# Kernel tuning notes

Hardware: AMD Instinct MI355X
Metric: run time of the kernel (lower is better)

## Reference

```python
import jax, jax.numpy as jnp
import numpy as np

NUM_NODES = 1_000_000
D_IN = 128
D_OUT = 128
NUM_REL = 16          # relations; +1 for self-connection relation
BATCH = 16384
NUM_SAMPLE = 32


def setup_inputs() -> dict:
    key = jax.random.key(0)
    k1, k2, k3, k4 = jax.random.split(key, 4)
    embed_table = jax.random.normal(k1, (NUM_NODES, D_IN), dtype=jnp.float32)
    # per-relation weight: [R+1, size_out, size_in], xavier-ish scale
    relation_weights = jax.random.normal(k2, (NUM_REL + 1, D_OUT, D_IN), dtype=jnp.float32)
    relation_weights = relation_weights * jnp.sqrt(2.0 / (D_IN + D_OUT))
    sampled_neighbors = jax.random.randint(k3, (BATCH, NUM_SAMPLE), 0, NUM_NODES, dtype=jnp.int64)
    sampled_relations = jax.random.randint(k4, (BATCH, NUM_SAMPLE), 0, NUM_REL + 1, dtype=jnp.int64)
    return {
        "embed_table": embed_table,
        "relation_weights": relation_weights,
        "sampled_neighbors": sampled_neighbors,
        "sampled_relations": sampled_relations,
    }


def reference(embed_table, relation_weights, sampled_neighbors, sampled_relations):
    # Gather sampled neighbor embeddings: [N, S, D]
    emb = embed_table[sampled_neighbors]
    num_sample = emb.shape[1]
    num_rel_p1 = relation_weights.shape[0]
    # One-hot relation mask [N, S, R+1]; aggregated = mean over S of (emb * onehot)
    # Equivalent einsum avoids materializing the [N, S, R+1, D] intermediate.
    onehot = jax.nn.one_hot(sampled_relations, num_rel_p1, dtype=emb.dtype)
    agg = jnp.einsum("nsr,nsd->nrd", onehot, emb) / num_sample  # [N, R+1, D]
    # Per-relation matmul (bmm over R+1) then mean over relations.
    # relation_weights: [R+1, O, I]; agg: [N, R+1, I] -> [N, O]
    out = jnp.einsum("nri,roi->no", agg, relation_weights) / num_rel_p1
    return jax.nn.relu(out * 1000.0)
```

## Files before the change

### kernel.cpp

```cpp
#include <hip/hip_runtime.h>

constexpr int D     = 128;
constexpr int R1    = 17;
constexpr int BATCH = 16384;
constexpr int S     = 32;
constexpr int K     = R1 * D;
constexpr int KB    = K / 8;
constexpr int NPB   = 16;
constexpr int AS    = K + 8;
constexpr int THREADS = 512;

typedef __attribute__((ext_vector_type(8))) short short8;
typedef __attribute__((ext_vector_type(4))) float f32x4;

__device__ __forceinline__ unsigned short f2bf_u(float f) {
    union { float f; unsigned u; } c; c.f = f;
    unsigned u = c.u;
    u += 0x7fffu + ((u >> 16) & 1u);
    return (unsigned short)(u >> 16);
}

__device__ __forceinline__ unsigned pack2bf(float lo, float hi) {
    return (unsigned)f2bf_u(lo) | ((unsigned)f2bf_u(hi) << 16);
}

__global__ void pack_w_kernel(const float* __restrict__ W, short* __restrict__ Bp) {
    int tid = blockIdx.x * 256 + threadIdx.x;
    if (tid >= R1 * D * D) return;
    int og = tid / K;
    int k  = tid - og * K;
    int r = k >> 7, i = k & 127;
    float v = W[((size_t)r * D + og) * D + i];
    int ot = og >> 4, o = og & 15, kb = k >> 3, j = k & 7;
    Bp[(((size_t)ot * KB + kb) * 16 + o) * 8 + j] = (short)f2bf_u(v);
}

#define ACC_SWITCH(r, x)                                              \
    switch (r) {                                                      \
        case 0:  a0.x  += x.x; a0.y  += x.y; break;                   \
        case 1:  a1.x  += x.x; a1.y  += x.y; break;                   \
        case 2:  a2.x  += x.x; a2.y  += x.y; break;                   \
        case 3:  a3.x  += x.x; a3.y  += x.y; break;                   \
        case 4:  a4.x  += x.x; a4.y  += x.y; break;                   \
        case 5:  a5.x  += x.x; a5.y  += x.y; break;                   \
        case 6:  a6.x  += x.x; a6.y  += x.y; break;                   \
        case 7:  a7.x  += x.x; a7.y  += x.y; break;                   \
        case 8:  a8.x  += x.x; a8.y  += x.y; break;                   \
        case 9:  a9.x  += x.x; a9.y  += x.y; break;                   \
        case 10: a10.x += x.x; a10.y += x.y; break;                   \
        case 11: a11.x += x.x; a11.y += x.y; break;                   \
        case 12: a12.x += x.x; a12.y += x.y; break;                   \
        case 13: a13.x += x.x; a13.y += x.y; break;                   \
        case 14: a14.x += x.x; a14.y += x.y; break;                   \
        case 15: a15.x += x.x; a15.y += x.y; break;                   \
        default: a16.x += x.x; a16.y += x.y; break;                   \
    }

__global__ __launch_bounds__(THREADS, 4)
void rgcn_kernel(const float* __restrict__ embed,
                 const short* __restrict__ Bp,
                 const int*   __restrict__ nbrs,
                 const int*   __restrict__ rels,
                 float* __restrict__ out)
{
    __shared__ short agg16[NPB][AS];

    const int t     = threadIdx.x;
    const int lane  = t & 63;
    const int w     = t >> 6;
    const int node0 = blockIdx.x * NPB;

    #pragma unroll 1
    for (int p = 0; p < 2; ++p) {
        const int nl = w * 2 + p;
        const int gn = node0 + nl;
        int my;
        if (lane < 32) my = nbrs[(size_t)gn * S + lane];
        else           my = rels[(size_t)gn * S + (lane - 32)];

        float2 a0={0,0},a1={0,0},a2={0,0},a3={0,0},a4={0,0},a5={0,0},
               a6={0,0},a7={0,0},a8={0,0},a9={0,0},a10={0,0},a11={0,0},
               a12={0,0},a13={0,0},a14={0,0},a15={0,0},a16={0,0};

        #pragma unroll 1
        for (int c = 0; c < 2; ++c) {
            const int sbase = c * 16;
            float2 v[16];
            #pragma unroll
            for (int j = 0; j < 16; ++j) {
                const int idx = __builtin_amdgcn_readlane(my, sbase + j);
                v[j] = *reinterpret_cast<const float2*>(embed + (size_t)idx * D + 2 * lane);
            }
            #pragma unroll
            for (int j = 0; j < 16; ++j) {
                const int r = __builtin_amdgcn_readlane(my, 32 + sbase + j);
                const float2 x = v[j];
                ACC_SWITCH(r, x)
            }
        }

        unsigned* arow = reinterpret_cast<unsigned*>(&agg16[nl][2 * lane]);
        arow[0*64]  = pack2bf(a0.x,  a0.y);   arow[1*64]  = pack2bf(a1.x,  a1.y);
        arow[2*64]  = pack2bf(a2.x,  a2.y);   arow[3*64]  = pack2bf(a3.x,  a3.y);
        arow[4*64]  = pack2bf(a4.x,  a4.y);   arow[5*64]  = pack2bf(a5.x,  a5.y);
        arow[6*64]  = pack2bf(a6.x,  a6.y);   arow[7*64]  = pack2bf(a7.x,  a7.y);
        arow[8*64]  = pack2bf(a8.x,  a8.y);   arow[9*64]  = pack2bf(a9.x,  a9.y);
        arow[10*64] = pack2bf(a10.x, a10.y);  arow[11*64] = pack2bf(a11.x, a11.y);
        arow[12*64] = pack2bf(a12.x, a12.y);  arow[13*64] = pack2bf(a13.x, a13.y);
        arow[14*64] = pack2bf(a14.x, a14.y);  arow[15*64] = pack2bf(a15.x, a15.y);
        arow[16*64] = pack2bf(a16.x, a16.y);
    }
    __syncthreads();

    {
        const int m   = lane & 15;
        const int kb4 = lane >> 4;

        f32x4 acc = {0.f, 0.f, 0.f, 0.f};

        const short* ar = &agg16[m][kb4 * 8];
        const short* bb = Bp + (((size_t)w * KB + kb4) * 16 + m) * 8;

        #pragma unroll 4
        for (int step = 0; step < K / 32; ++step) {
            const short8 a = *reinterpret_cast<const short8*>(ar + step * 32);
            const short8 b = *reinterpret_cast<const short8*>(bb + (size_t)step * 512);
            acc = __builtin_amdgcn_mfma_f32_16x16x32_bf16(a, b, acc, 0, 0, 0);
        }

        const float sc = 1000.0f / (float)(S * R1);
        #pragma unroll
        for (int j = 0; j < 4; ++j) {
            const int node = kb4 * 4 + j;
            out[(size_t)(node0 + node) * D + w * 16 + m] = fmaxf(acc[j] * sc, 0.0f);
        }
    }
}

extern "C" void kernel_launch(void* const* d_in, const int* in_sizes, int n_in,
                              void* d_out, int out_size, void* d_ws, size_t ws_size,
                              hipStream_t stream) {
    const float* embed = (const float*)d_in[0];
    const float* W     = (const float*)d_in[1];
    const int*   nbrs  = (const int*)d_in[2];
    const int*   rels  = (const int*)d_in[3];
    float* out = (float*)d_out;
    short* Bp  = (short*)d_ws;

    hipLaunchKernelGGL(pack_w_kernel, dim3((R1 * D * D + 255) / 256), dim3(256), 0, stream,
                       W, Bp);
    hipLaunchKernelGGL(rgcn_kernel, dim3(BATCH / NPB), dim3(THREADS), 0, stream,
                       embed, Bp, nbrs, rels, out);
}
```

Measured before the change: 80.52 us.

## Split fused RGCN into separate aggregation and GEMM kernels via workspace

Splits the fused gather-aggregate-matmul kernel into an aggregation kernel that writes bf16 per-relation aggregates to workspace and a GEMM kernel that tiles 32 nodes per block. Each stage gets its own occupancy and launch configuration, and the GEMM reuses each weight fragment across two row tiles. This adds a global round trip of about 71 MB of intermediate data and an extra launch. The fused path is kept as a fallback when the workspace is too small.

```diff
diff --git a/kernel.cpp b/kernel.cpp
--- a/kernel.cpp
+++ b/kernel.cpp
@@ -1,4 +1,5 @@
 #include <hip/hip_runtime.h>
+#include <hip/hip_bf16.h>
 
 constexpr int D     = 128;
 constexpr int R1    = 17;
@@ -6,9 +7,10 @@
 constexpr int S     = 32;
 constexpr int K     = R1 * D;
 constexpr int KB    = K / 8;
-constexpr int NPB   = 16;
-constexpr int AS    = K + 8;
-constexpr int THREADS = 512;
+
+constexpr size_t BP_BYTES  = (size_t)R1 * D * D * 2;
+constexpr size_t AGG_OFF   = BP_BYTES;
+constexpr size_t AGG_BYTES = (size_t)BATCH * K * 2;
 
 typedef __attribute__((ext_vector_type(8))) short short8;
 typedef __attribute__((ext_vector_type(4))) float f32x4;
@@ -19,7 +21,6 @@
     u += 0x7fffu + ((u >> 16) & 1u);
     return (unsigned short)(u >> 16);
 }
-
 __device__ __forceinline__ unsigned pack2bf(float lo, float hi) {
     return (unsigned)f2bf_u(lo) | ((unsigned)f2bf_u(hi) << 16);
 }
@@ -56,20 +57,112 @@
         default: a16.x += x.x; a16.y += x.y; break;                   \
     }
 
-__global__ __launch_bounds__(THREADS, 4)
-void rgcn_kernel(const float* __restrict__ embed,
+__global__ __launch_bounds__(256, 6)
+void agg_kernel(const float* __restrict__ embed,
+                const int*   __restrict__ nbrs,
+                const int*   __restrict__ rels,
+                short*       __restrict__ Ag)
+{
+    const int t    = threadIdx.x;
+    const int lane = t & 63;
+    const int w    = t >> 6;
+    const int gn   = blockIdx.x * 4 + w;
+
+    int my;
+    if (lane < 32) my = nbrs[(size_t)gn * S + lane];
+    else           my = rels[(size_t)gn * S + (lane - 32)];
+
+    float2 a0={0,0},a1={0,0},a2={0,0},a3={0,0},a4={0,0},a5={0,0},
+           a6={0,0},a7={0,0},a8={0,0},a9={0,0},a10={0,0},a11={0,0},
+           a12={0,0},a13={0,0},a14={0,0},a15={0,0},a16={0,0};
+
+    #pragma unroll 1
+    for (int c = 0; c < 4; ++c) {
+        const int sbase = c * 8;
+        float2 v[8];
+        #pragma unroll
+        for (int j = 0; j < 8; ++j) {
+            const int idx = __builtin_amdgcn_readlane(my, sbase + j);
+            v[j] = *reinterpret_cast<const float2*>(embed + (size_t)idx * D + 2 * lane);
+        }
+        #pragma unroll
+        for (int j = 0; j < 8; ++j) {
+            const int r = __builtin_amdgcn_readlane(my, 32 + sbase + j);
+            const float2 x = v[j];
+            ACC_SWITCH(r, x)
+        }
+    }
+
+    unsigned* orow = reinterpret_cast<unsigned*>(Ag + (size_t)gn * K);
+    orow[0*64+lane]  = pack2bf(a0.x,  a0.y);   orow[1*64+lane]  = pack2bf(a1.x,  a1.y);
+    orow[2*64+lane]  = pack2bf(a2.x,  a2.y);   orow[3*64+lane]  = pack2bf(a3.x,  a3.y);
+    orow[4*64+lane]  = pack2bf(a4.x,  a4.y);   orow[5*64+lane]  = pack2bf(a5.x,  a5.y);
+    orow[6*64+lane]  = pack2bf(a6.x,  a6.y);   orow[7*64+lane]  = pack2bf(a7.x,  a7.y);
+    orow[8*64+lane]  = pack2bf(a8.x,  a8.y);   orow[9*64+lane]  = pack2bf(a9.x,  a9.y);
+    orow[10*64+lane] = pack2bf(a10.x, a10.y);  orow[11*64+lane] = pack2bf(a11.x, a11.y);
+    orow[12*64+lane] = pack2bf(a12.x, a12.y);  orow[13*64+lane] = pack2bf(a13.x, a13.y);
+    orow[14*64+lane] = pack2bf(a14.x, a14.y);  orow[15*64+lane] = pack2bf(a15.x, a15.y);
+    orow[16*64+lane] = pack2bf(a16.x, a16.y);
+}
+
+constexpr int BM  = 32;
+constexpr int AS2 = K + 8;
+
+__global__ __launch_bounds__(512, 1)
+void gemm_kernel(const short* __restrict__ Ag,
                  const short* __restrict__ Bp,
-                 const int*   __restrict__ nbrs,
-                 const int*   __restrict__ rels,
                  float* __restrict__ out)
 {
-    __shared__ short agg16[NPB][AS];
+    __shared__ short At[BM][AS2];
 
     const int t     = threadIdx.x;
     const int lane  = t & 63;
     const int w     = t >> 6;
-    const int node0 = blockIdx.x * NPB;
-
+    const int node0 = blockIdx.x * BM;
+
+    #pragma unroll
+    for (int rr = 0; rr < 4; ++rr) {
+        const int row = w * 4 + rr;
+        const int4* src = reinterpret_cast<const int4*>(Ag + (size_t)(node0 + row) * K);
+        int4* dst = reinterpret_cast<int4*>(&At[row][0]);
+        for (int c = lane; c < K / 8; c += 64)
+            dst[c] = src[c];
+    }
+    __syncthreads();
+
+    const int m   = lane & 15;
+    const int kb4 = lane >> 4;
+    const short* bb = Bp + (((size_t)w * KB + kb4) * 16 + m) * 8;
+    const float sc = 1000.0f / (float)(S * R1);
+
+    #pragma unroll 1
+    for (int ms = 0; ms < 2; ++ms) {
+        const short* ar = &At[ms * 16 + m][kb4 * 8];
+        f32x4 acc = {0.f, 0.f, 0.f, 0.f};
+        #pragma unroll 4
+        for (int step = 0; step < K / 32; ++step) {
+            const short8 a = *reinterpret_cast<const short8*>(ar + step * 32);
+            const short8 b = *reinterpret_cast<const short8*>(bb + (size_t)step * 512);
+            acc = __builtin_amdgcn_mfma_f32_16x16x32_bf16(a, b, acc, 0, 0, 0);
+        }
+        #pragma unroll
+        for (int j = 0; j < 4; ++j) {
+            out[(size_t)(node0 + ms * 16 + kb4 * 4 + j) * D + w * 16 + m] =
+                fmaxf(acc[j] * sc, 0.0f);
+        }
+    }
+}
+
+constexpr int NPBF = 16;
+constexpr int ASF  = K + 8;
+__global__ __launch_bounds__(512, 4)
+void rgcn_fused(const float* __restrict__ embed, const short* __restrict__ Bp,
+                const int* __restrict__ nbrs, const int* __restrict__ rels,
+                float* __restrict__ out)
+{
+    __shared__ short agg16[NPBF][ASF];
+    const int t = threadIdx.x, lane = t & 63, w = t >> 6;
+    const int node0 = blockIdx.x * NPBF;
     #pragma unroll 1
     for (int p = 0; p < 2; ++p) {
         const int nl = w * 2 + p;
@@ -77,11 +170,9 @@
         int my;
         if (lane < 32) my = nbrs[(size_t)gn * S + lane];
         else           my = rels[(size_t)gn * S + (lane - 32)];
-
         float2 a0={0,0},a1={0,0},a2={0,0},a3={0,0},a4={0,0},a5={0,0},
                a6={0,0},a7={0,0},a8={0,0},a9={0,0},a10={0,0},a11={0,0},
                a12={0,0},a13={0,0},a14={0,0},a15={0,0},a16={0,0};
-
         #pragma unroll 1
         for (int c = 0; c < 2; ++c) {
             const int sbase = c * 16;
@@ -98,42 +189,33 @@
                 ACC_SWITCH(r, x)
             }
         }
-
         unsigned* arow = reinterpret_cast<unsigned*>(&agg16[nl][2 * lane]);
-        arow[0*64]  = pack2bf(a0.x,  a0.y);   arow[1*64]  = pack2bf(a1.x,  a1.y);
-        arow[2*64]  = pack2bf(a2.x,  a2.y);   arow[3*64]  = pack2bf(a3.x,  a3.y);
-        arow[4*64]  = pack2bf(a4.x,  a4.y);   arow[5*64]  = pack2bf(a5.x,  a5.y);
-        arow[6*64]  = pack2bf(a6.x,  a6.y);   arow[7*64]  = pack2bf(a7.x,  a7.y);
-        arow[8*64]  = pack2bf(a8.x,  a8.y);   arow[9*64]  = pack2bf(a9.x,  a9.y);
-        arow[10*64] = pack2bf(a10.x, a10.y);  arow[11*64] = pack2bf(a11.x, a11.y);
-        arow[12*64] = pack2bf(a12.x, a12.y);  arow[13*64] = pack2bf(a13.x, a13.y);
-        arow[14*64] = pack2bf(a14.x, a14.y);  arow[15*64] = pack2bf(a15.x, a15.y);
-        arow[16*64] = pack2bf(a16.x, a16.y);
+        arow[0*64]=pack2bf(a0.x,a0.y);   arow[1*64]=pack2bf(a1.x,a1.y);
+        arow[2*64]=pack2bf(a2.x,a2.y);   arow[3*64]=pack2bf(a3.x,a3.y);
+        arow[4*64]=pack2bf(a4.x,a4.y);   arow[5*64]=pack2bf(a5.x,a5.y);
+        arow[6*64]=pack2bf(a6.x,a6.y);   arow[7*64]=pack2bf(a7.x,a7.y);
+        arow[8*64]=pack2bf(a8.x,a8.y);   arow[9*64]=pack2bf(a9.x,a9.y);
+        arow[10*64]=pack2bf(a10.x,a10.y);arow[11*64]=pack2bf(a11.x,a11.y);
+        arow[12*64]=pack2bf(a12.x,a12.y);arow[13*64]=pack2bf(a13.x,a13.y);
+        arow[14*64]=pack2bf(a14.x,a14.y);arow[15*64]=pack2bf(a15.x,a15.y);
+        arow[16*64]=pack2bf(a16.x,a16.y);
     }
     __syncthreads();
-
     {
-        const int m   = lane & 15;
-        const int kb4 = lane >> 4;
-
-        f32x4 acc = {0.f, 0.f, 0.f, 0.f};
-
+        const int m = lane & 15, kb4 = lane >> 4;
+        f32x4 acc = {0.f,0.f,0.f,0.f};
         const short* ar = &agg16[m][kb4 * 8];
         const short* bb = Bp + (((size_t)w * KB + kb4) * 16 + m) * 8;
-
         #pragma unroll 4
         for (int step = 0; step < K / 32; ++step) {
             const short8 a = *reinterpret_cast<const short8*>(ar + step * 32);
             const short8 b = *reinterpret_cast<const short8*>(bb + (size_t)step * 512);
             acc = __builtin_amdgcn_mfma_f32_16x16x32_bf16(a, b, acc, 0, 0, 0);
         }
-
         const float sc = 1000.0f / (float)(S * R1);
         #pragma unroll
-        for (int j = 0; j < 4; ++j) {
-            const int node = kb4 * 4 + j;
-            out[(size_t)(node0 + node) * D + w * 16 + m] = fmaxf(acc[j] * sc, 0.0f);
-        }
+        for (int j = 0; j < 4; ++j)
+            out[(size_t)(node0 + kb4 * 4 + j) * D + w * 16 + m] = fmaxf(acc[j] * sc, 0.0f);
     }
 }
 
@@ -149,6 +231,15 @@
 
     hipLaunchKernelGGL(pack_w_kernel, dim3((R1 * D * D + 255) / 256), dim3(256), 0, stream,
                        W, Bp);
-    hipLaunchKernelGGL(rgcn_kernel, dim3(BATCH / NPB), dim3(THREADS), 0, stream,
-                       embed, Bp, nbrs, rels, out);
-}
+
+    if (ws_size >= AGG_OFF + AGG_BYTES) {
+        short* Ag = (short*)((char*)d_ws + AGG_OFF);
+        hipLaunchKernelGGL(agg_kernel, dim3(BATCH / 4), dim3(256), 0, stream,
+                           embed, nbrs, rels, Ag);
+        hipLaunchKernelGGL(gemm_kernel, dim3(BATCH / BM), dim3(512), 0, stream,
+                           Ag, Bp, out);
+    } else {
+        hipLaunchKernelGGL(rgcn_fused, dim3(BATCH / NPBF), dim3(512), 0, stream,
+                           embed, Bp, nbrs, rels, out);
+    }
+}
```

Result: slower. 138.0 us (+71.4%).

## Split block into producer gather waves and consumer MFMA waves with double buffering

Applied to the files above, without the earlier changes.

Each block now handles four groups of 16 nodes with 1024 threads. Eight waves gather and aggregate neighbor embeddings for the next group into one of two LDS buffers while the other eight run the MFMA GEMM on the current group. This is meant to overlap the memory-bound gather with the matmul. In exchange there are fewer, larger blocks, LDS use doubles, and a block-wide barrier is needed per group. Half the waves sit idle during the prologue and the last group.

```diff
diff --git a/kernel.cpp b/kernel.cpp
--- a/kernel.cpp
+++ b/kernel.cpp
@@ -7,8 +7,10 @@
 constexpr int K     = R1 * D;
 constexpr int KB    = K / 8;
 constexpr int NPB   = 16;
+constexpr int NGRP  = 4;
 constexpr int AS    = K + 8;
-constexpr int THREADS = 512;
+constexpr int THREADS = 1024;
+constexpr int GRID  = BATCH / (NPB * NGRP);
 
 typedef __attribute__((ext_vector_type(8))) short short8;
 typedef __attribute__((ext_vector_type(4))) float f32x4;
@@ -19,7 +21,6 @@
     u += 0x7fffu + ((u >> 16) & 1u);
     return (unsigned short)(u >> 16);
 }
-
 __device__ __forceinline__ unsigned pack2bf(float lo, float hi) {
     return (unsigned)f2bf_u(lo) | ((unsigned)f2bf_u(hi) << 16);
 }
@@ -35,105 +36,125 @@
     Bp[(((size_t)ot * KB + kb) * 16 + o) * 8 + j] = (short)f2bf_u(v);
 }
 
-#define ACC_SWITCH(r, x)                                              \
-    switch (r) {                                                      \
-        case 0:  a0.x  += x.x; a0.y  += x.y; break;                   \
-        case 1:  a1.x  += x.x; a1.y  += x.y; break;                   \
-        case 2:  a2.x  += x.x; a2.y  += x.y; break;                   \
-        case 3:  a3.x  += x.x; a3.y  += x.y; break;                   \
-        case 4:  a4.x  += x.x; a4.y  += x.y; break;                   \
-        case 5:  a5.x  += x.x; a5.y  += x.y; break;                   \
-        case 6:  a6.x  += x.x; a6.y  += x.y; break;                   \
-        case 7:  a7.x  += x.x; a7.y  += x.y; break;                   \
-        case 8:  a8.x  += x.x; a8.y  += x.y; break;                   \
-        case 9:  a9.x  += x.x; a9.y  += x.y; break;                   \
-        case 10: a10.x += x.x; a10.y += x.y; break;                   \
-        case 11: a11.x += x.x; a11.y += x.y; break;                   \
-        case 12: a12.x += x.x; a12.y += x.y; break;                   \
-        case 13: a13.x += x.x; a13.y += x.y; break;                   \
-        case 14: a14.x += x.x; a14.y += x.y; break;                   \
-        case 15: a15.x += x.x; a15.y += x.y; break;                   \
-        default: a16.x += x.x; a16.y += x.y; break;                   \
+#define ACC_SWITCH(rr_, vv_)                                          \
+    switch (rr_) {                                                    \
+        case 0:  a0.x  += vv_.x; a0.y  += vv_.y; break;               \
+        case 1:  a1.x  += vv_.x; a1.y  += vv_.y; break;               \
+        case 2:  a2.x  += vv_.x; a2.y  += vv_.y; break;               \
+        case 3:  a3.x  += vv_.x; a3.y  += vv_.y; break;               \
+        case 4:  a4.x  += vv_.x; a4.y  += vv_.y; break;               \
+        case 5:  a5.x  += vv_.x; a5.y  += vv_.y; break;               \
+        case 6:  a6.x  += vv_.x; a6.y  += vv_.y; break;               \
+        case 7:  a7.x  += vv_.x; a7.y  += vv_.y; break;               \
+        case 8:  a8.x  += vv_.x; a8.y  += vv_.y; break;               \
+        case 9:  a9.x  += vv_.x; a9.y  += vv_.y; break;               \
+        case 10: a10.x += vv_.x; a10.y += vv_.y; break;               \
+        case 11: a11.x += vv_.x; a11.y += vv_.y; break;               \
+        case 12: a12.x += vv_.x; a12.y += vv_.y; break;               \
+        case 13: a13.x += vv_.x; a13.y += vv_.y; break;               \
+        case 14: a14.x += vv_.x; a14.y += vv_.y; break;               \
+        case 15: a15.x += vv_.x; a15.y += vv_.y; break;               \
+        default: a16.x += vv_.x; a16.y += vv_.y; break;               \
     }
 
+__device__ __forceinline__ void gather_one(const float* __restrict__ embed,
+                                           const int*   __restrict__ nbrs,
+                                           const int*   __restrict__ rels,
+                                           int gn, int lane, short* row)
+{
+    int my;
+    if (lane < 32) my = nbrs[(size_t)gn * S + lane];
+    else           my = rels[(size_t)gn * S + (lane - 32)];
+
+    float2 a0={0,0},a1={0,0},a2={0,0},a3={0,0},a4={0,0},a5={0,0},
+           a6={0,0},a7={0,0},a8={0,0},a9={0,0},a10={0,0},a11={0,0},
+           a12={0,0},a13={0,0},a14={0,0},a15={0,0},a16={0,0};
+
+    #pragma unroll 1
+    for (int c = 0; c < 2; ++c) {
+        const int sbase = c * 16;
+        float2 v[16];
+        #pragma unroll
+        for (int j = 0; j < 16; ++j) {
+            const int idx = __builtin_amdgcn_readlane(my, sbase + j);
+            v[j] = *reinterpret_cast<const float2*>(embed + (size_t)idx * D + 2 * lane);
+        }
+        #pragma unroll
+        for (int j = 0; j < 16; ++j) {
+            const int r = __builtin_amdgcn_readlane(my, 32 + sbase + j);
+            const float2 vx = v[j];
+            ACC_SWITCH(r, vx)
+        }
+    }
+
+    unsigned* arow_ = reinterpret_cast<unsigned*>(row) + lane;
+    arow_[0*64]  = pack2bf(a0.x,  a0.y);   arow_[1*64]  = pack2bf(a1.x,  a1.y);
+    arow_[2*64]  = pack2bf(a2.x,  a2.y);   arow_[3*64]  = pack2bf(a3.x,  a3.y);
+    arow_[4*64]  = pack2bf(a4.x,  a4.y);   arow_[5*64]  = pack2bf(a5.x,  a5.y);
+    arow_[6*64]  = pack2bf(a6.x,  a6.y);   arow_[7*64]  = pack2bf(a7.x,  a7.y);
+    arow_[8*64]  = pack2bf(a8.x,  a8.y);   arow_[9*64]  = pack2bf(a9.x,  a9.y);
+    arow_[10*64] = pack2bf(a10.x, a10.y);  arow_[11*64] = pack2bf(a11.x, a11.y);
+    arow_[12*64] = pack2bf(a12.x, a12.y);  arow_[13*64] = pack2bf(a13.x, a13.y);
+    arow_[14*64] = pack2bf(a14.x, a14.y);  arow_[15*64] = pack2bf(a15.x, a15.y);
+    arow_[16*64] = pack2bf(a16.x, a16.y);
+}
+
 __global__ __launch_bounds__(THREADS, 4)
-void rgcn_kernel(const float* __restrict__ embed,
-                 const short* __restrict__ Bp,
-                 const int*   __restrict__ nbrs,
-                 const int*   __restrict__ rels,
-                 float* __restrict__ out)
+void rgcn_pc_kernel(const float* __restrict__ embed,
+                    const short* __restrict__ Bp,
+                    const int*   __restrict__ nbrs,
+                    const int*   __restrict__ rels,
+                    float* __restrict__ out)
 {
-    __shared__ short agg16[NPB][AS];
+    __shared__ short At[2][NPB][AS];
 
     const int t     = threadIdx.x;
     const int lane  = t & 63;
     const int w     = t >> 6;
-    const int node0 = blockIdx.x * NPB;
+    const int base0 = blockIdx.x * NGRP * NPB;
 
-    #pragma unroll 1
-    for (int p = 0; p < 2; ++p) {
-        const int nl = w * 2 + p;
-        const int gn = node0 + nl;
-        int my;
-        if (lane < 32) my = nbrs[(size_t)gn * S + lane];
-        else           my = rels[(size_t)gn * S + (lane - 32)];
-
-        float2 a0={0,0},a1={0,0},a2={0,0},a3={0,0},a4={0,0},a5={0,0},
-               a6={0,0},a7={0,0},a8={0,0},a9={0,0},a10={0,0},a11={0,0},
-               a12={0,0},a13={0,0},a14={0,0},a15={0,0},a16={0,0};
-
+    if (w < 8) {
         #pragma unroll 1
-        for (int c = 0; c < 2; ++c) {
-            const int sbase = c * 16;
-            float2 v[16];
-            #pragma unroll
-            for (int j = 0; j < 16; ++j) {
-                const int idx = __builtin_amdgcn_readlane(my, sbase + j);
-                v[j] = *reinterpret_cast<const float2*>(embed + (size_t)idx * D + 2 * lane);
-            }
-            #pragma unroll
-            for (int j = 0; j < 16; ++j) {
-                const int r = __builtin_amdgcn_readlane(my, 32 + sbase + j);
-                const float2 x = v[j];
-                ACC_SWITCH(r, x)
-            }
-        }
-
-        unsigned* arow = reinterpret_cast<unsigned*>(&agg16[nl][2 * lane]);
-        arow[0*64]  = pack2bf(a0.x,  a0.y);   arow[1*64]  = pack2bf(a1.x,  a1.y);
-        arow[2*64]  = pack2bf(a2.x,  a2.y);   arow[3*64]  = pack2bf(a3.x,  a3.y);
-        arow[4*64]  = pack2bf(a4.x,  a4.y);   arow[5*64]  = pack2bf(a5.x,  a5.y);
-        arow[6*64]  = pack2bf(a6.x,  a6.y);   arow[7*64]  = pack2bf(a7.x,  a7.y);
-        arow[8*64]  = pack2bf(a8.x,  a8.y);   arow[9*64]  = pack2bf(a9.x,  a9.y);
-        arow[10*64] = pack2bf(a10.x, a10.y);  arow[11*64] = pack2bf(a11.x, a11.y);
-        arow[12*64] = pack2bf(a12.x, a12.y);  arow[13*64] = pack2bf(a13.x, a13.y);
-        arow[14*64] = pack2bf(a14.x, a14.y);  arow[15*64] = pack2bf(a15.x, a15.y);
-        arow[16*64] = pack2bf(a16.x, a16.y);
+        for (int p = 0; p < 2; ++p)
+            gather_one(embed, nbrs, rels, base0 + 2 * w + p, lane, &At[0][2 * w + p][0]);
     }
     __syncthreads();
 
-    {
-        const int m   = lane & 15;
-        const int kb4 = lane >> 4;
+    #pragma unroll 1
+    for (int g = 0; g < NGRP; ++g) {
+        if (w < 8) {
+            if (g + 1 < NGRP) {
+                const int nb = base0 + (g + 1) * NPB;
+                #pragma unroll 1
+                for (int p = 0; p < 2; ++p)
+                    gather_one(embed, nbrs, rels, nb + 2 * w + p, lane,
+                               &At[(g + 1) & 1][2 * w + p][0]);
+            }
+        } else {
+            const int cw  = w - 8;
+            const int m   = lane & 15;
+            const int kb4 = lane >> 4;
 
-        f32x4 acc = {0.f, 0.f, 0.f, 0.f};
+            f32x4 acc = {0.f, 0.f, 0.f, 0.f};
+            const short* ar = &At[g & 1][m][kb4 * 8];
+            const short* bb = Bp + (((size_t)cw * KB + kb4) * 16 + m) * 8;
 
-        const short* ar = &agg16[m][kb4 * 8];
-        const short* bb = Bp + (((size_t)w * KB + kb4) * 16 + m) * 8;
+            #pragma unroll 4
+            for (int step = 0; step < K / 32; ++step) {
+                const short8 a = *reinterpret_cast<const short8*>(ar + step * 32);
+                const short8 b = *reinterpret_cast<const short8*>(bb + (size_t)step * 512);
+                acc = __builtin_amdgcn_mfma_f32_16x16x32_bf16(a, b, acc, 0, 0, 0);
+            }
 
-        #pragma unroll 4
-        for (int step = 0; step < K / 32; ++step) {
-            const short8 a = *reinterpret_cast<const short8*>(ar + step * 32);
-            const short8 b = *reinterpret_cast<const short8*>(bb + (size_t)step * 512);
-            acc = __builtin_amdgcn_mfma_f32_16x16x32_bf16(a, b, acc, 0, 0, 0);
+            const float sc = 1000.0f / (float)(S * R1);
+            const int nbase = base0 + g * NPB;
+            #pragma unroll
+            for (int j = 0; j < 4; ++j) {
+                out[(size_t)(nbase + kb4 * 4 + j) * D + cw * 16 + m] =
+                    fmaxf(acc[j] * sc, 0.0f);
+            }
         }
-
-        const float sc = 1000.0f / (float)(S * R1);
-        #pragma unroll
-        for (int j = 0; j < 4; ++j) {
-            const int node = kb4 * 4 + j;
-            out[(size_t)(node0 + node) * D + w * 16 + m] = fmaxf(acc[j] * sc, 0.0f);
-        }
+        __syncthreads();
     }
 }
 
@@ -149,6 +170,6 @@
 
     hipLaunchKernelGGL(pack_w_kernel, dim3((R1 * D * D + 255) / 256), dim3(256), 0, stream,
                        W, Bp);
-    hipLaunchKernelGGL(rgcn_kernel, dim3(BATCH / NPB), dim3(THREADS), 0, stream,
+    hipLaunchKernelGGL(rgcn_pc_kernel, dim3(GRID), dim3(THREADS), 0, stream,
                        embed, Bp, nbrs, rels, out);
 }
```

Measured after the change: 97.50 us. +21.1%, slower.
